# Optimization experiments

Hardware: AMD Instinct MI355X
Metric: run time of the kernel (lower is better)

Reference implementation:

```python
import jax, jax.numpy as jnp
import numpy as np

N, E, D = 100000, 600000, 128

def setup_inputs() -> dict:
    key = jax.random.key(0)
    ks = jax.random.split(key, 6)
    s = 1.0 / np.sqrt(D)
    return {
        "h": jax.random.normal(ks[0], (N, D), dtype=jnp.float32),
        "edge_index": jax.random.randint(ks[1], (2, E), 0, N, dtype=jnp.int64),
        "Wg": jax.random.normal(ks[2], (2 * D, D), dtype=jnp.float32) * s,
        "bg": jnp.zeros((D,), dtype=jnp.float32),
        "Ws": jax.random.normal(ks[3], (D, D), dtype=jnp.float32) * s,
        "bs": jnp.zeros((D,), dtype=jnp.float32),
        "Wr": jax.random.normal(ks[4], (D, D), dtype=jnp.float32) * s,
        "br": jnp.zeros((D,), dtype=jnp.float32),
    }

def reference(h, edge_index, Wg, bg, Ws, bs, Wr, br):
    send, rec = edge_index[0], edge_index[1]
    h_rec = h[rec]            # [E, D]
    h_send = h[send]          # [E, D]
    # gate: sigmoid(Linear(cat([h_rec, h_send])))  -- split W to avoid concat copy
    gate_in = h_rec @ Wg[:h.shape[1]] + h_send @ Wg[h.shape[1]:] + bg
    eta = jax.nn.sigmoid(gate_in)                      # [E, D]
    h_messages = eta * (h_send @ Ws + bs)              # [E, D]
    h_agg = jax.ops.segment_sum(h_messages, rec, num_segments=h.shape[0])
    return (h @ Wr + br) + h_agg
```

## Files before the change

### kernel.cpp

```cpp
#include <hip/hip_runtime.h>
#include <stdint.h>

#define FD 128

typedef __bf16 bf16x8 __attribute__((ext_vector_type(8)));
typedef unsigned short u16x8 __attribute__((ext_vector_type(8)));
typedef float  f32x16 __attribute__((ext_vector_type(16)));

__device__ __forceinline__ unsigned short f2bf(float f) {
    unsigned u = __float_as_uint(f);
    unsigned r = u + 0x7fffu + ((u >> 16) & 1u);
    return (unsigned short)(r >> 16);
}
__device__ __forceinline__ float bflo(unsigned u) { return __uint_as_float(u << 16); }
__device__ __forceinline__ float bfhi(unsigned u) { return __uint_as_float(u & 0xffff0000u); }

__global__ __launch_bounds__(256) void prep_kernel(
    const float* __restrict__ Wg,
    const float* __restrict__ Ws,
    const float* __restrict__ Wr,
    unsigned short* __restrict__ Wf)
{
    int wid = blockIdx.x * 256 + threadIdx.x;
    if (wid >= 512 * 128) return;
    int j  = wid & 7;
    int l  = (wid >> 3) & 63;
    int kt = (wid >> 9) & 7;
    int ct = wid >> 12;
    int k  = kt * 16 + (l >> 5) * 8 + j;
    int c  = ct * 32 + (l & 31);
    float v;
    if (c < 128)      v = Wg[k * FD + c];
    else if (c < 256) v = Wg[(128 + k) * FD + (c - 128)];
    else if (c < 384) v = Ws[k * FD + (c - 256)];
    else              v = Wr[k * FD + (c - 384)];
    Wf[wid] = f2bf(v);
}

__global__ __launch_bounds__(256, 4) void gemm_kernel(
    const float* __restrict__ h,
    const unsigned short* __restrict__ Wf,
    const float* __restrict__ bg,
    const float* __restrict__ bs,
    const float* __restrict__ br,
    unsigned short* __restrict__ A,
    unsigned short* __restrict__ B,
    unsigned short* __restrict__ S,
    float* __restrict__ out,
    int N)
{
    __shared__ unsigned short Bsh[16384];

    const int w    = blockIdx.y;
    const int lane = threadIdx.x & 63;
    const int wid  = threadIdx.x >> 6;

    {
        const unsigned short* src = Wf + (size_t)w * 16384 + (size_t)threadIdx.x * 8;
        unsigned short* dst = Bsh + (size_t)threadIdx.x * 8;
        #pragma unroll
        for (int p = 0; p < 8; ++p) {
            __builtin_amdgcn_global_load_lds(
                (const __attribute__((address_space(1))) void*)(src + p * 2048),
                (__attribute__((address_space(3))) void*)(dst + p * 2048),
                16, 0, 0);
        }
    }

    const int col_l  = lane & 31;
    const int rhalf  = (lane >> 5) * 4;
    float bias[4];
    #pragma unroll
    for (int i = 0; i < 4; ++i) {
        int col = i * 32 + col_l;
        bias[i] = (w == 0) ? bg[col] : (w == 2) ? bs[col] : (w == 3) ? br[col] : 0.0f;
    }

    __syncthreads();

    const int stride = gridDim.x * 128;
    for (int rb0 = blockIdx.x * 128; rb0 < N; rb0 += stride) {
        const int rb = rb0 + wid * 32;
        int arow = rb + (lane & 31);
        if (arow >= N) arow = N - 1;
        const float* aptr = h + (size_t)arow * FD + (lane >> 5) * 8;

        bf16x8 afrag[8];
        #pragma unroll
        for (int kt = 0; kt < 8; ++kt) {
            float4 f0 = *(const float4*)(aptr + kt * 16);
            float4 f1 = *(const float4*)(aptr + kt * 16 + 4);
            union { u16x8 u; bf16x8 b; } cv;
            cv.u[0] = f2bf(f0.x); cv.u[1] = f2bf(f0.y);
            cv.u[2] = f2bf(f0.z); cv.u[3] = f2bf(f0.w);
            cv.u[4] = f2bf(f1.x); cv.u[5] = f2bf(f1.y);
            cv.u[6] = f2bf(f1.z); cv.u[7] = f2bf(f1.w);
            afrag[kt] = cv.b;
        }

        f32x16 acc[4];
        #pragma unroll
        for (int i = 0; i < 4; ++i)
            #pragma unroll
            for (int r = 0; r < 16; ++r) acc[i][r] = 0.0f;

        #pragma unroll
        for (int kt = 0; kt < 8; ++kt) {
            #pragma unroll
            for (int i = 0; i < 4; ++i) {
                bf16x8 bfr = *(const bf16x8*)(Bsh + (size_t)((i * 8 + kt) * 64 + lane) * 8);
                acc[i] = __builtin_amdgcn_mfma_f32_32x32x16_bf16(
                             afrag[kt], bfr, acc[i], 0, 0, 0);
            }
        }

        if (rb + 32 <= N) {
            #pragma unroll
            for (int i = 0; i < 4; ++i) {
                int col = i * 32 + col_l;
                #pragma unroll
                for (int r = 0; r < 16; ++r) {
                    int row = rb + (r & 3) + 8 * (r >> 2) + rhalf;
                    float v = acc[i][r] + bias[i];
                    size_t off = (size_t)row * FD + col;
                    if (w == 0)      A[off] = f2bf(v);
                    else if (w == 1) B[off] = f2bf(v);
                    else if (w == 2) S[off] = f2bf(v);
                    else             out[off] = v;
                }
            }
        } else {
            #pragma unroll
            for (int i = 0; i < 4; ++i) {
                int col = i * 32 + col_l;
                #pragma unroll
                for (int r = 0; r < 16; ++r) {
                    int row = rb + (r & 3) + 8 * (r >> 2) + rhalf;
                    if (row < N) {
                        float v = acc[i][r] + bias[i];
                        size_t off = (size_t)row * FD + col;
                        if (w == 0)      A[off] = f2bf(v);
                        else if (w == 1) B[off] = f2bf(v);
                        else if (w == 2) S[off] = f2bf(v);
                        else             out[off] = v;
                    }
                }
            }
        }
    }
}

__global__ __launch_bounds__(256) void hist_kernel(
    const int* __restrict__ idx, int* __restrict__ deg, int E)
{
    int e = blockIdx.x * 256 + threadIdx.x;
    if (e >= E) return;
    atomicAdd(&deg[idx[E + e]], 1);
}

__global__ __launch_bounds__(256) void scan1_kernel(
    const int* __restrict__ deg, int* __restrict__ partial, int N)
{
    __shared__ int sh[256];
    int base = blockIdx.x * 1024 + threadIdx.x * 4;
    int s = 0;
    #pragma unroll
    for (int j = 0; j < 4; ++j) s += (base + j < N) ? deg[base + j] : 0;
    sh[threadIdx.x] = s;
    __syncthreads();
    for (int ofs = 128; ofs > 0; ofs >>= 1) {
        if (threadIdx.x < ofs) sh[threadIdx.x] += sh[threadIdx.x + ofs];
        __syncthreads();
    }
    if (threadIdx.x == 0) partial[blockIdx.x] = sh[0];
}

__global__ __launch_bounds__(256) void scan2_kernel(int* __restrict__ partial, int nb)
{
    __shared__ int sh[256];
    int t = threadIdx.x;
    int p = (t < nb) ? partial[t] : 0;
    sh[t] = p;
    __syncthreads();
    for (int ofs = 1; ofs < 256; ofs <<= 1) {
        int x = (t >= ofs) ? sh[t - ofs] : 0;
        __syncthreads();
        sh[t] += x;
        __syncthreads();
    }
    if (t < nb) partial[t] = sh[t] - p;
}

__global__ __launch_bounds__(256) void scan3_kernel(
    int* __restrict__ deg, const int* __restrict__ partial, int N)
{
    __shared__ int sh[256];
    int base = blockIdx.x * 1024 + threadIdx.x * 4;
    int v[4];
    #pragma unroll
    for (int j = 0; j < 4; ++j) v[j] = (base + j < N) ? deg[base + j] : 0;
    int tsum = v[0] + v[1] + v[2] + v[3];
    sh[threadIdx.x] = tsum;
    __syncthreads();
    for (int ofs = 1; ofs < 256; ofs <<= 1) {
        int x = (threadIdx.x >= ofs) ? sh[threadIdx.x - ofs] : 0;
        __syncthreads();
        sh[threadIdx.x] += x;
        __syncthreads();
    }
    int run = partial[blockIdx.x] + sh[threadIdx.x] - tsum;
    #pragma unroll
    for (int j = 0; j < 4; ++j) {
        if (base + j < N) deg[base + j] = run;
        run += v[j];
    }
}

__global__ __launch_bounds__(256) void scatter_kernel(
    const int* __restrict__ idx, int* __restrict__ off,
    int* __restrict__ csr, int E)
{
    int e = blockIdx.x * 256 + threadIdx.x;
    if (e >= E) return;
    int s = idx[e];
    int r = idx[E + e];
    int pos = atomicAdd(&off[r], 1);
    csr[pos] = s;
}

__global__ __launch_bounds__(256) void aggregate_kernel(
    const int* __restrict__ off,
    const int* __restrict__ csr,
    const unsigned* __restrict__ A,
    const unsigned* __restrict__ B,
    const unsigned* __restrict__ S,
    float* __restrict__ out,
    int N)
{
    int r = blockIdx.x * 4 + (threadIdx.x >> 6);
    if (r >= N) return;
    int lane = threadIdx.x & 63;

    int start = (r == 0) ? 0 : off[r - 1];
    int end   = off[r];
    if (start >= end) return;

    unsigned ua = A[(size_t)r * 64 + lane];
    float a0 = bflo(ua), a1 = bfhi(ua);
    float acc0 = 0.0f, acc1 = 0.0f;

    int i = start;
    for (; i + 1 < end; i += 2) {
        int s0 = csr[i], s1 = csr[i + 1];
        unsigned ub0 = B[(size_t)s0 * 64 + lane];
        unsigned us0 = S[(size_t)s0 * 64 + lane];
        unsigned ub1 = B[(size_t)s1 * 64 + lane];
        unsigned us1 = S[(size_t)s1 * 64 + lane];
        float g00 = a0 + bflo(ub0), g01 = a1 + bfhi(ub0);
        float g10 = a0 + bflo(ub1), g11 = a1 + bfhi(ub1);
        acc0 += bflo(us0) * __builtin_amdgcn_rcpf(1.0f + __expf(-g00));
        acc1 += bfhi(us0) * __builtin_amdgcn_rcpf(1.0f + __expf(-g01));
        acc0 += bflo(us1) * __builtin_amdgcn_rcpf(1.0f + __expf(-g10));
        acc1 += bfhi(us1) * __builtin_amdgcn_rcpf(1.0f + __expf(-g11));
    }
    if (i < end) {
        int s0 = csr[i];
        unsigned ub0 = B[(size_t)s0 * 64 + lane];
        unsigned us0 = S[(size_t)s0 * 64 + lane];
        float g00 = a0 + bflo(ub0), g01 = a1 + bfhi(ub0);
        acc0 += bflo(us0) * __builtin_amdgcn_rcpf(1.0f + __expf(-g00));
        acc1 += bfhi(us0) * __builtin_amdgcn_rcpf(1.0f + __expf(-g01));
    }

    float2* o = (float2*)(out + (size_t)r * FD + 2 * lane);
    float2 cur = *o;
    cur.x += acc0;
    cur.y += acc1;
    *o = cur;
}

extern "C" void kernel_launch(void* const* d_in, const int* in_sizes, int n_in,
                              void* d_out, int out_size, void* d_ws, size_t ws_size,
                              hipStream_t stream)
{
    const float* h  = (const float*)d_in[0];
    const int*   ei = (const int*)d_in[1];
    const float* Wg = (const float*)d_in[2];
    const float* bg = (const float*)d_in[3];
    const float* Ws = (const float*)d_in[4];
    const float* bs = (const float*)d_in[5];
    const float* Wr = (const float*)d_in[6];
    const float* br = (const float*)d_in[7];
    float* out = (float*)d_out;

    const int N = in_sizes[0] / FD;
    const int E = in_sizes[1] / 2;

    unsigned short* Wf  = (unsigned short*)d_ws;
    unsigned short* Abf = Wf + 512 * FD;
    unsigned short* Bbf = Abf + (size_t)N * FD;
    unsigned short* Sbf = Bbf + (size_t)N * FD;
    int* deg     = (int*)(Sbf + (size_t)N * FD);
    int* partial = deg + N;
    int* csr     = partial + 256;

    size_t need = (size_t)(512 * FD + 3ull * N * FD) * 2 + ((size_t)N + 256 + E) * 4;
    if (ws_size < need) return;

    const int nb = (N + 1023) / 1024;
    if (nb > 256) return;

    hipMemsetAsync(deg, 0, (size_t)N * 4, stream);

    prep_kernel<<<(512 * FD + 255) / 256, 256, 0, stream>>>(Wg, Ws, Wr, Wf);
    dim3 ggrid(256, 4);
    gemm_kernel<<<ggrid, 256, 0, stream>>>(h, Wf, bg, bs, br,
                                           Abf, Bbf, Sbf, out, N);
    hist_kernel<<<(E + 255) / 256, 256, 0, stream>>>(ei, deg, E);
    scan1_kernel<<<nb, 256, 0, stream>>>(deg, partial, N);
    scan2_kernel<<<1, 256, 0, stream>>>(partial, nb);
    scan3_kernel<<<nb, 256, 0, stream>>>(deg, partial, N);
    scatter_kernel<<<(E + 255) / 256, 256, 0, stream>>>(ei, deg, csr, E);
    aggregate_kernel<<<(N + 3) / 4, 256, 0, stream>>>(deg, csr,
                                                      (const unsigned*)Abf,
                                                      (const unsigned*)Bbf,
                                                      (const unsigned*)Sbf,
                                                      out, N);
}
```

Before: 307.8 us.

## Pack bf16 projection outputs into 8-byte stores and unroll edge gather by four

The GEMM epilogue for the A, B and S projections now packs the four bf16 values a lane holds for one row into a single 8-byte store. Previously these were written as scattered 2-byte stores. This permutes the feature columns inside the bf16 intermediates. The aggregation kernel decodes that permutation when it adds into the fp32 output, and its edge-gather loop is unrolled to four edges so more loads are in flight. The cost is that the final read-modify-write to the output is now two scattered scalar accesses instead of one float2 access.

```diff
diff --git a/kernel.cpp b/kernel.cpp
--- a/kernel.cpp
+++ b/kernel.cpp
@@ -14,6 +14,7 @@
 }
 __device__ __forceinline__ float bflo(unsigned u) { return __uint_as_float(u << 16); }
 __device__ __forceinline__ float bfhi(unsigned u) { return __uint_as_float(u & 0xffff0000u); }
+
 
 __global__ __launch_bounds__(256) void prep_kernel(
     const float* __restrict__ Wg,
@@ -75,6 +76,7 @@
         int col = i * 32 + col_l;
         bias[i] = (w == 0) ? bg[col] : (w == 2) ? bs[col] : (w == 3) ? br[col] : 0.0f;
     }
+    unsigned short* dstABS = (w == 0) ? A : (w == 1) ? B : S;
 
     __syncthreads();
 
@@ -114,36 +116,29 @@
             }
         }
 
-        if (rb + 32 <= N) {
+        const bool interior = (rb + 32 <= N);
+        if (w == 3) {
             #pragma unroll
             for (int i = 0; i < 4; ++i) {
                 int col = i * 32 + col_l;
                 #pragma unroll
                 for (int r = 0; r < 16; ++r) {
                     int row = rb + (r & 3) + 8 * (r >> 2) + rhalf;
-                    float v = acc[i][r] + bias[i];
-                    size_t off = (size_t)row * FD + col;
-                    if (w == 0)      A[off] = f2bf(v);
-                    else if (w == 1) B[off] = f2bf(v);
-                    else if (w == 2) S[off] = f2bf(v);
-                    else             out[off] = v;
+                    if (interior || row < N)
+                        out[(size_t)row * FD + col] = acc[i][r] + bias[i];
                 }
             }
         } else {
             #pragma unroll
-            for (int i = 0; i < 4; ++i) {
-                int col = i * 32 + col_l;
-                #pragma unroll
-                for (int r = 0; r < 16; ++r) {
-                    int row = rb + (r & 3) + 8 * (r >> 2) + rhalf;
-                    if (row < N) {
-                        float v = acc[i][r] + bias[i];
-                        size_t off = (size_t)row * FD + col;
-                        if (w == 0)      A[off] = f2bf(v);
-                        else if (w == 1) B[off] = f2bf(v);
-                        else if (w == 2) S[off] = f2bf(v);
-                        else             out[off] = v;
-                    }
+            for (int r = 0; r < 16; ++r) {
+                int row = rb + (r & 3) + 8 * (r >> 2) + rhalf;
+                if (interior || row < N) {
+                    uint2 pk;
+                    pk.x = (unsigned)f2bf(acc[0][r] + bias[0])
+                         | ((unsigned)f2bf(acc[1][r] + bias[1]) << 16);
+                    pk.y = (unsigned)f2bf(acc[2][r] + bias[2])
+                         | ((unsigned)f2bf(acc[3][r] + bias[3]) << 16);
+                    *(uint2*)(dstABS + (size_t)row * FD + col_l * 4) = pk;
                 }
             }
         }
@@ -250,33 +245,37 @@
     float acc0 = 0.0f, acc1 = 0.0f;
 
     int i = start;
-    for (; i + 1 < end; i += 2) {
-        int s0 = csr[i], s1 = csr[i + 1];
+    for (; i + 3 < end; i += 4) {
+        int s0 = csr[i], s1 = csr[i + 1], s2 = csr[i + 2], s3 = csr[i + 3];
         unsigned ub0 = B[(size_t)s0 * 64 + lane];
         unsigned us0 = S[(size_t)s0 * 64 + lane];
         unsigned ub1 = B[(size_t)s1 * 64 + lane];
         unsigned us1 = S[(size_t)s1 * 64 + lane];
-        float g00 = a0 + bflo(ub0), g01 = a1 + bfhi(ub0);
-        float g10 = a0 + bflo(ub1), g11 = a1 + bfhi(ub1);
-        acc0 += bflo(us0) * __builtin_amdgcn_rcpf(1.0f + __expf(-g00));
-        acc1 += bfhi(us0) * __builtin_amdgcn_rcpf(1.0f + __expf(-g01));
-        acc0 += bflo(us1) * __builtin_amdgcn_rcpf(1.0f + __expf(-g10));
-        acc1 += bfhi(us1) * __builtin_amdgcn_rcpf(1.0f + __expf(-g11));
-    }
-    if (i < end) {
+        unsigned ub2 = B[(size_t)s2 * 64 + lane];
+        unsigned us2 = S[(size_t)s2 * 64 + lane];
+        unsigned ub3 = B[(size_t)s3 * 64 + lane];
+        unsigned us3 = S[(size_t)s3 * 64 + lane];
+        acc0 += bflo(us0) * __builtin_amdgcn_rcpf(1.0f + __expf(-(a0 + bflo(ub0))));
+        acc1 += bfhi(us0) * __builtin_amdgcn_rcpf(1.0f + __expf(-(a1 + bfhi(ub0))));
+        acc0 += bflo(us1) * __builtin_amdgcn_rcpf(1.0f + __expf(-(a0 + bflo(ub1))));
+        acc1 += bfhi(us1) * __builtin_amdgcn_rcpf(1.0f + __expf(-(a1 + bfhi(ub1))));
+        acc0 += bflo(us2) * __builtin_amdgcn_rcpf(1.0f + __expf(-(a0 + bflo(ub2))));
+        acc1 += bfhi(us2) * __builtin_amdgcn_rcpf(1.0f + __expf(-(a1 + bfhi(ub2))));
+        acc0 += bflo(us3) * __builtin_amdgcn_rcpf(1.0f + __expf(-(a0 + bflo(ub3))));
+        acc1 += bfhi(us3) * __builtin_amdgcn_rcpf(1.0f + __expf(-(a1 + bfhi(ub3))));
+    }
+    for (; i < end; ++i) {
         int s0 = csr[i];
         unsigned ub0 = B[(size_t)s0 * 64 + lane];
         unsigned us0 = S[(size_t)s0 * 64 + lane];
-        float g00 = a0 + bflo(ub0), g01 = a1 + bfhi(ub0);
-        acc0 += bflo(us0) * __builtin_amdgcn_rcpf(1.0f + __expf(-g00));
-        acc1 += bfhi(us0) * __builtin_amdgcn_rcpf(1.0f + __expf(-g01));
-    }
-
-    float2* o = (float2*)(out + (size_t)r * FD + 2 * lane);
-    float2 cur = *o;
-    cur.x += acc0;
-    cur.y += acc1;
-    *o = cur;
+        acc0 += bflo(us0) * __builtin_amdgcn_rcpf(1.0f + __expf(-(a0 + bflo(ub0))));
+        acc1 += bfhi(us0) * __builtin_amdgcn_rcpf(1.0f + __expf(-(a1 + bfhi(ub0))));
+    }
+
+    int f0 = (lane >> 1) + 64 * (lane & 1);
+    float* o = out + (size_t)r * FD;
+    o[f0]      += acc0;
+    o[f0 + 32] += acc1;
 }
 
 extern "C" void kernel_launch(void* const* d_in, const int* in_sizes, int n_in,
```

Result: slower. 382.1 us (+24.2%).
